# Kernel optimization log

Hardware: AMD Instinct MI355X
Metric: run time of the kernel (lower is better)

## Reference

```python
import jax, jax.numpy as jnp
import numpy as np

B, N, H, L = 4, 200, 128, 3
HH = H // 2
VOC_E_IN, VOC_E_OUT, NODE_DIM = 3, 2, 2
EPS_BN = 1e-5


def masked_bn(x, m, gamma, beta):
    """BatchNorm1d (batch stats, no running stats) applied only to masked positions.
    x: (..., H), m: (...) float mask. Unmasked entries pass through unchanged."""
    mm = m[..., None]
    cnt = jnp.sum(m)
    axes = tuple(range(x.ndim - 1))
    mean = jnp.sum(x * mm, axis=axes) / cnt
    var = jnp.sum(((x - mean) ** 2) * mm, axis=axes) / cnt  # biased, as BatchNorm1d
    xn = (x - mean) * jax.lax.rsqrt(var + EPS_BN) * gamma + beta
    return jnp.where(mm > 0, xn, x)


def gcn_layer(x, e, mask, sq_mask, p, i):
    # EdgeFeatures: e_ij = U*e_ij + V*x_i + V*x_j (V*x masked)
    Ue = jnp.einsum('bijh,hk->bijk', e, p['eU_w'][i]) + p['eU_b'][i]
    Vx_e = mask[..., None] * (jnp.einsum('bnh,hk->bnk', x, p['eV_w'][i]) + p['eV_b'][i])
    e_tmp = Ue + Vx_e[:, :, None, :] + Vx_e[:, None, :, :]
    gate = jax.nn.sigmoid(e_tmp)
    # NodeFeatures (mean aggregation)
    Ux = mask[..., None] * (jnp.einsum('bnh,hk->bnk', x, p['nU_w'][i]) + p['nU_b'][i])
    Vx = mask[..., None] * (jnp.einsum('bnh,hk->bnk', x, p['nV_w'][i]) + p['nV_b'][i])
    gate_m = gate * sq_mask[..., None]
    agg = jnp.einsum('bijh,bjh->bih', gate_m, Vx)
    denom = jnp.sum(gate_m, axis=2)
    x_tmp = Ux + agg / (1e-20 + denom)
    # masked batchnorm + ReLU + residual
    e_bn = masked_bn(e_tmp, sq_mask, p['bnE_g'][i], p['bnE_b'][i])
    x_bn = masked_bn(x_tmp, mask, p['bnN_g'][i], p['bnN_b'][i])
    return x + jax.nn.relu(x_bn), e + jax.nn.relu(e_bn)


def forward(x_edges, x_edges_values, x_nodes_coord, mask, p):
    x = jnp.einsum('bnd,dh->bnh', x_nodes_coord, p['w_coord'])          # (B,N,H)
    e_val = x_edges_values[..., None] * p['w_eval'][0]                  # (B,N,N,HH)
    e_tag = p['emb_edge'][x_edges]                                      # (B,N,N,HH)
    e = jnp.concatenate([e_val, e_tag], axis=-1)                        # (B,N,N,H)
    sq_mask = mask[:, :, None] * mask[:, None, :]
    for i in range(L):
        x, e = gcn_layer(x, e, mask, sq_mask, p, i)
    # MLP on edges (mlp_layers=2 -> one hidden ReLU layer)
    h = jax.nn.relu(jnp.einsum('bijh,hk->bijk', e, p['mlp_U_w']) + p['mlp_U_b'])
    y = jnp.einsum('bijh,hk->bijk', h, p['mlp_V_w']) + p['mlp_V_b']     # (B,N,N,2)
    return y


def setup_inputs() -> dict:
    key = jax.random.key(0)
    ks = jax.random.split(key, 32)
    x_edges = jax.random.randint(ks[0], (B, N, N), 0, VOC_E_IN)
    x_edges_values = jax.random.uniform(ks[1], (B, N, N), dtype=jnp.float32)
    x_nodes_coord = jax.random.uniform(ks[2], (B, N, NODE_DIM), dtype=jnp.float32)
    # prefix mask: variable graph sizes padded to N (as ConvTSP builds)
    lens = jax.random.randint(ks[3], (B,), N // 2, N + 1)
    mask = (jnp.arange(N)[None, :] < lens[:, None]).astype(jnp.float32)
    s = 1.0 / np.sqrt(H)
    inp = dict(x_edges=x_edges, x_edges_values=x_edges_values,
               x_nodes_coord=x_nodes_coord, mask=mask,
               w_coord=jax.random.normal(ks[4], (NODE_DIM, H)) * 0.5,
               w_eval=jax.random.normal(ks[5], (1, HH)) * 0.5,
               emb_edge=jax.random.normal(ks[6], (VOC_E_IN, HH)) * 0.5,
               eU_w=jax.random.normal(ks[7], (L, H, H)) * s,
               eU_b=jnp.zeros((L, H)),
               eV_w=jax.random.normal(ks[8], (L, H, H)) * s,
               eV_b=jnp.zeros((L, H)),
               nU_w=jax.random.normal(ks[9], (L, H, H)) * s,
               nU_b=jnp.zeros((L, H)),
               nV_w=jax.random.normal(ks[10], (L, H, H)) * s,
               nV_b=jnp.zeros((L, H)),
               bnE_g=jnp.ones((L, H)), bnE_b=jnp.zeros((L, H)),
               bnN_g=jnp.ones((L, H)), bnN_b=jnp.zeros((L, H)),
               mlp_U_w=jax.random.normal(ks[11], (H, H)) * s,
               mlp_U_b=jnp.zeros((H,)),
               mlp_V_w=jax.random.normal(ks[12], (H, VOC_E_OUT)) * s,
               mlp_V_b=jnp.zeros((VOC_E_OUT,)))
    return inp


def reference(x_edges, x_edges_values, x_nodes_coord, mask,
              w_coord, w_eval, emb_edge,
              eU_w, eU_b, eV_w, eV_b, nU_w, nU_b, nV_w, nV_b,
              bnE_g, bnE_b, bnN_g, bnN_b,
              mlp_U_w, mlp_U_b, mlp_V_w, mlp_V_b):
    p = dict(w_coord=w_coord, w_eval=w_eval, emb_edge=emb_edge,
             eU_w=eU_w, eU_b=eU_b, eV_w=eV_w, eV_b=eV_b,
             nU_w=nU_w, nU_b=nU_b, nV_w=nV_w, nV_b=nV_b,
             bnE_g=bnE_g, bnE_b=bnE_b, bnN_g=bnN_g, bnN_b=bnN_b,
             mlp_U_w=mlp_U_w, mlp_U_b=mlp_U_b, mlp_V_w=mlp_V_w, mlp_V_b=mlp_V_b)
    return forward(x_edges, x_edges_values, x_nodes_coord, mask, p)
```

## Files before the change

kernel.cpp:

```cpp
#include <hip/hip_runtime.h>
#include <hip/hip_bf16.h>


typedef __hip_bfloat16 bf16;
typedef __attribute__((ext_vector_type(8))) short short8_t;
typedef __attribute__((ext_vector_type(4))) float f32x4;

#define B_ 4
#define N_ 200
#define H_ 128
#define BN_ (B_ * N_)
#define MT_ 13
#define MROWS_ 208

__device__ __forceinline__ unsigned short f2b(float f) {
  unsigned int i = __float_as_uint(f);
  i = (i + 0x7fffu + ((i >> 16) & 1u)) >> 16;
  return (unsigned short)i;
}
__device__ __forceinline__ float b2f16(unsigned short u) {
  return __uint_as_float((unsigned int)u << 16);
}


__global__ __launch_bounds__(128) void k_init_x(
    const float* __restrict__ coord, const float* __restrict__ w_coord,
    float* __restrict__ x) {
  int bi = blockIdx.x, h = threadIdx.x;
  float c0 = coord[bi * 2 + 0], c1 = coord[bi * 2 + 1];
  x[(size_t)bi * H_ + h] = c0 * w_coord[h] + c1 * w_coord[H_ + h];
}

__global__ __launch_bounds__(256) void k_cnt(const float* __restrict__ mask,
                                             float* __restrict__ cnts) {
  int t = threadIdx.x, b = t >> 6, l = t & 63;
  float s = 0.f;
  for (int n = l; n < N_; n += 64) s += mask[b * N_ + n];
#pragma unroll
  for (int d = 1; d < 64; d <<= 1) s += __shfl_xor(s, d);
  __shared__ float ms[B_];
  if (l == 0) ms[b] = s;
  __syncthreads();
  if (t == 0) {
    float cn = 0.f, ce = 0.f;
    for (int k = 0; k < B_; ++k) { cn += ms[k]; ce += ms[k] * ms[k]; }
    cnts[0] = cn; cnts[1] = ce;
  }
}

__global__ __launch_bounds__(256) void k_prep_w(const float* __restrict__ eUw,
                                                const float* __restrict__ mUw,
                                                bf16* __restrict__ WT) {
  int blk = blockIdx.x;
  const float* src = (blk < 3) ? (eUw + (size_t)blk * H_ * H_) : mUw;
  bf16* dst = WT + (size_t)blk * H_ * H_;
  for (int q = threadIdx.x; q < H_ * H_; q += 256) {
    int out = q >> 7, in = q & 127;
    dst[q] = __float2bfloat16(src[in * H_ + out]);
  }
}


template <int UPD>
__global__ __launch_bounds__(128) void k_node_lin(
    float* __restrict__ x, const float* __restrict__ xtmp,
    const float* __restrict__ sumsPrev, const float* __restrict__ cnts,
    const float* __restrict__ gNp, const float* __restrict__ bNp,
    const float* __restrict__ eVw, const float* __restrict__ eVb,
    const float* __restrict__ nUw, const float* __restrict__ nUb,
    const float* __restrict__ nVw, const float* __restrict__ nVb,
    const float* __restrict__ mask, float* __restrict__ Vxe,
    float* __restrict__ Ux, float* __restrict__ Vx) {
  __shared__ float xr[H_];
  int bi = blockIdx.x, h = threadIdx.x;
  float m = mask[bi];
  float xv = x[(size_t)bi * H_ + h];
  if (UPD) {
    float cntN = cnts[0];
    float mN = sumsPrev[256 + h] / cntN;
    float vN = sumsPrev[384 + h] / cntN - mN * mN;
    float scN = gNp[h] * rsqrtf(vN + 1e-5f);
    float shN = bNp[h] - mN * scN;
    float tv = xtmp[(size_t)bi * H_ + h];
    float xn = (m > 0.f) ? fmaf(tv, scN, shN) : tv;
    xv += fmaxf(xn, 0.f);
    x[(size_t)bi * H_ + h] = xv;
  }
  xr[h] = xv;
  __syncthreads();
  float a = 0.f, bvv = 0.f, c = 0.f;
#pragma unroll 4
  for (int k = 0; k < H_; ++k) {
    float kx = xr[k];
    a   = fmaf(kx, eVw[k * H_ + h], a);
    bvv = fmaf(kx, nUw[k * H_ + h], bvv);
    c   = fmaf(kx, nVw[k * H_ + h], c);
  }
  Vxe[(size_t)bi * H_ + h] = m * (a + eVb[h]);
  Ux[(size_t)bi * H_ + h]  = m * (bvv + nUb[h]);
  Vx[(size_t)bi * H_ + h]  = m * (c + nVb[h]);
}


template <int MODE, bool DO_X>
__global__ __launch_bounds__(256, 3) void k_edge(
    bf16* __restrict__ e, bf16* __restrict__ etmp,
    const float* __restrict__ sumsPrev, const float* __restrict__ cnts,
    const float* __restrict__ gEp, const float* __restrict__ bEp,
    const int* __restrict__ xe, const float* __restrict__ ev,
    const float* __restrict__ w_eval, const float* __restrict__ emb,
    const bf16* __restrict__ WT, const float* __restrict__ eUb,
    const float* __restrict__ Vxe, const float* __restrict__ Vx,
    const float* __restrict__ Ux, const float* __restrict__ mask,
    float* __restrict__ xtmp, float* __restrict__ sumsCur) {
  __shared__ __align__(16) char sA[MROWS_ * 256];
  __shared__ float ssE_s[256];
  const int bi = blockIdx.x;
  const int b = bi / N_;
  const int t = threadIdx.x;
  const int lane = t & 63;
  const int w = t >> 6;
  const float mask_i = mask[bi];

  if (MODE != 0) {
    int h = t & 127;
    float cntE = cnts[1];
    float mE = sumsPrev[h] / cntE;
    float vE = sumsPrev[128 + h] / cntE - mE * mE;
    float scE = gEp[h] * rsqrtf(vE + 1e-5f);
    ssE_s[t] = (t < 128) ? scE : (bEp[h] - mE * scE);
    __syncthreads();
  }

  const int colA = (w << 5) + (lane & 15);
  const int colB = colA + 16;
  const int kgrp = (lane >> 4) << 3;
  const short* wp0 = (const short*)WT + colA * H_ + kgrp;
  const short* wp1 = (const short*)WT + colB * H_ + kgrp;
  short8_t bfA0 = *(const short8_t*)(wp0);
  short8_t bfA1 = *(const short8_t*)(wp0 + 32);
  short8_t bfA2 = *(const short8_t*)(wp0 + 64);
  short8_t bfA3 = *(const short8_t*)(wp0 + 96);
  short8_t bfB0 = *(const short8_t*)(wp1);
  short8_t bfB1 = *(const short8_t*)(wp1 + 32);
  short8_t bfB2 = *(const short8_t*)(wp1 + 64);
  short8_t bfB3 = *(const short8_t*)(wp1 + 96);

  {
    unsigned short* eb = (unsigned short*)e + (size_t)bi * N_ * H_;
    const unsigned short* tb =
        (const unsigned short*)etmp + (size_t)bi * N_ * H_;
    for (int q4 = t; q4 < MROWS_ * 32; q4 += 256) {
      int row = q4 >> 5, k0 = (q4 & 31) << 2;
      float v0 = 0.f, v1 = 0.f, v2 = 0.f, v3 = 0.f;
      if (row < N_) {
        if (MODE == 0 || MODE == 2) {
          if (k0 < 64) {
            float evv = ev[bi * N_ + row];
            float4 we = *(const float4*)(w_eval + k0);
            v0 = evv * we.x; v1 = evv * we.y;
            v2 = evv * we.z; v3 = evv * we.w;
          } else {
            float4 em4 = *(const float4*)(emb + xe[bi * N_ + row] * 64 + (k0 - 64));
            v0 = em4.x; v1 = em4.y; v2 = em4.z; v3 = em4.w;
          }
        } else {
          ushort4 e4 = *(const ushort4*)(eb + row * H_ + k0);
          v0 = b2f16(e4.x); v1 = b2f16(e4.y);
          v2 = b2f16(e4.z); v3 = b2f16(e4.w);
        }
        if (MODE != 0) {
          ushort4 t4 = *(const ushort4*)(tb + row * H_ + k0);
          float mj = mask[b * N_ + row];
          bool msk = (mask_i * mj) > 0.f;
          float sc0 = ssE_s[k0 + 0], sc1 = ssE_s[k0 + 1];
          float sc2 = ssE_s[k0 + 2], sc3 = ssE_s[k0 + 3];
          float sh0 = ssE_s[128 + k0 + 0], sh1 = ssE_s[128 + k0 + 1];
          float sh2 = ssE_s[128 + k0 + 2], sh3 = ssE_s[128 + k0 + 3];
          float f0 = b2f16(t4.x), f1 = b2f16(t4.y);
          float f2 = b2f16(t4.z), f3 = b2f16(t4.w);
          v0 += fmaxf(msk ? fmaf(f0, sc0, sh0) : f0, 0.f);
          v1 += fmaxf(msk ? fmaf(f1, sc1, sh1) : f1, 0.f);
          v2 += fmaxf(msk ? fmaf(f2, sc2, sh2) : f2, 0.f);
          v3 += fmaxf(msk ? fmaf(f3, sc3, sh3) : f3, 0.f);
        }
      }
      unsigned int p0 = ((unsigned int)f2b(v1) << 16) | f2b(v0);
      unsigned int p1 = ((unsigned int)f2b(v3) << 16) | f2b(v2);
      if (MODE != 0 && row < N_)
        *(uint2*)(eb + row * H_ + k0) = make_uint2(p0, p1);
      unsigned long long pk = ((unsigned long long)p1 << 32) | p0;
      int byo = (row << 8) + ((k0 * 2) ^ ((row & 7) << 4));
      *(unsigned long long*)(sA + byo) = pk;
    }
  }
  __syncthreads();

  const float add0 = eUb[colA] + Vxe[(size_t)bi * H_ + colA];
  const float add1 = eUb[colB] + Vxe[(size_t)bi * H_ + colB];
  const float* VxeB = Vxe + (size_t)b * N_ * H_;
  const float* VxB  = Vx  + (size_t)b * N_ * H_;

  float agg0 = 0.f, agg1 = 0.f, den0 = 0.f, den1 = 0.f;
  float s1a = 0.f, s1b = 0.f, s2a = 0.f, s2b = 0.f;
  const int kb = (lane >> 4) << 4;

  for (int mt = 0; mt < MT_; ++mt) {
    f32x4 acc0 = {0.f, 0.f, 0.f, 0.f}, acc1 = {0.f, 0.f, 0.f, 0.f};
    int ra = (mt << 4) + (lane & 15);
    const char* ap = sA + (ra << 8);
    int sw = (ra & 7) << 4;
    short8_t av;
    av = *(const short8_t*)(ap + ((kb + 0) ^ sw));
    acc0 = __builtin_amdgcn_mfma_f32_16x16x32_bf16(av, bfA0, acc0, 0, 0, 0);
    acc1 = __builtin_amdgcn_mfma_f32_16x16x32_bf16(av, bfB0, acc1, 0, 0, 0);
    av = *(const short8_t*)(ap + ((kb + 64) ^ sw));
    acc0 = __builtin_amdgcn_mfma_f32_16x16x32_bf16(av, bfA1, acc0, 0, 0, 0);
    acc1 = __builtin_amdgcn_mfma_f32_16x16x32_bf16(av, bfB1, acc1, 0, 0, 0);
    av = *(const short8_t*)(ap + ((kb + 128) ^ sw));
    acc0 = __builtin_amdgcn_mfma_f32_16x16x32_bf16(av, bfA2, acc0, 0, 0, 0);
    acc1 = __builtin_amdgcn_mfma_f32_16x16x32_bf16(av, bfB2, acc1, 0, 0, 0);
    av = *(const short8_t*)(ap + ((kb + 192) ^ sw));
    acc0 = __builtin_amdgcn_mfma_f32_16x16x32_bf16(av, bfA3, acc0, 0, 0, 0);
    acc1 = __builtin_amdgcn_mfma_f32_16x16x32_bf16(av, bfB3, acc1, 0, 0, 0);
#pragma unroll
    for (int r = 0; r < 4; ++r) {
      int j = (mt << 4) + ((lane >> 4) << 2) + r;
      bool valid = (j < N_);
      float mj = valid ? mask[b * N_ + j] : 0.f;
      float sqm = mask_i * mj;
      float vj0 = valid ? VxeB[(size_t)j * H_ + colA] : 0.f;
      float vj1 = valid ? VxeB[(size_t)j * H_ + colB] : 0.f;
      float t0 = acc0[r] + add0 + vj0;
      float t1 = acc1[r] + add1 + vj1;
      if (valid) {
        size_t o = ((size_t)bi * N_ + j) * H_;
        ((unsigned short*)etmp)[o + colA] = f2b(t0);
        ((unsigned short*)etmp)[o + colB] = f2b(t1);
      }
      float g0 = sqm / (1.f + __expf(-t0));
      float g1 = sqm / (1.f + __expf(-t1));
      float vx0 = valid ? VxB[(size_t)j * H_ + colA] : 0.f;
      float vx1 = valid ? VxB[(size_t)j * H_ + colB] : 0.f;
      agg0 = fmaf(g0, vx0, agg0);
      agg1 = fmaf(g1, vx1, agg1);
      den0 += g0; den1 += g1;
      s1a = fmaf(t0, sqm, s1a);
      s1b = fmaf(t1, sqm, s1b);
      s2a = fmaf(t0 * sqm, t0, s2a);
      s2b = fmaf(t1 * sqm, t1, s2b);
    }
  }
#pragma unroll
  for (int d = 16; d <= 32; d <<= 1) {
    agg0 += __shfl_xor(agg0, d); agg1 += __shfl_xor(agg1, d);
    den0 += __shfl_xor(den0, d); den1 += __shfl_xor(den1, d);
    s1a += __shfl_xor(s1a, d);   s1b += __shfl_xor(s1b, d);
    s2a += __shfl_xor(s2a, d);   s2b += __shfl_xor(s2b, d);
  }
  if ((lane >> 4) == 0) {
    atomicAdd(&sumsCur[colA], s1a);
    atomicAdd(&sumsCur[colB], s1b);
    atomicAdd(&sumsCur[128 + colA], s2a);
    atomicAdd(&sumsCur[128 + colB], s2b);
    if (DO_X) {
      float xt0 = Ux[(size_t)bi * H_ + colA] + agg0 / (1e-20f + den0);
      float xt1 = Ux[(size_t)bi * H_ + colB] + agg1 / (1e-20f + den1);
      xtmp[(size_t)bi * H_ + colA] = xt0;
      xtmp[(size_t)bi * H_ + colB] = xt1;
      atomicAdd(&sumsCur[256 + colA], xt0 * mask_i);
      atomicAdd(&sumsCur[384 + colA], xt0 * xt0 * mask_i);
      atomicAdd(&sumsCur[256 + colB], xt1 * mask_i);
      atomicAdd(&sumsCur[384 + colB], xt1 * xt1 * mask_i);
    }
  }
}


__global__ __launch_bounds__(256, 2) void k_head(
    const bf16* __restrict__ e, const bf16* __restrict__ etmp,
    const float* __restrict__ sumsPrev, const float* __restrict__ cnts,
    const float* __restrict__ gEp, const float* __restrict__ bEp,
    const bf16* __restrict__ UT, const float* __restrict__ Ub,
    const float* __restrict__ Vw, const float* __restrict__ Vb,
    const float* __restrict__ mask, float* __restrict__ y) {
  __shared__ __align__(16) char sA[MROWS_ * 256];
  __shared__ float part[4][MROWS_][2];
  __shared__ float ssE_s[256];
  const int bi = blockIdx.x;
  const int b = bi / N_;
  const int t = threadIdx.x;
  const int lane = t & 63;
  const int w = t >> 6;
  const float mask_i = mask[bi];

  {
    int h = t & 127;
    float cntE = cnts[1];
    float mE = sumsPrev[h] / cntE;
    float vE = sumsPrev[128 + h] / cntE - mE * mE;
    float scE = gEp[h] * rsqrtf(vE + 1e-5f);
    ssE_s[t] = (t < 128) ? scE : (bEp[h] - mE * scE);
    __syncthreads();
  }

  const int colA = (w << 5) + (lane & 15);
  const int colB = colA + 16;
  const int kgrp = (lane >> 4) << 3;
  const short* wp0 = (const short*)UT + colA * H_ + kgrp;
  const short* wp1 = (const short*)UT + colB * H_ + kgrp;
  short8_t bfA0 = *(const short8_t*)(wp0);
  short8_t bfA1 = *(const short8_t*)(wp0 + 32);
  short8_t bfA2 = *(const short8_t*)(wp0 + 64);
  short8_t bfA3 = *(const short8_t*)(wp0 + 96);
  short8_t bfB0 = *(const short8_t*)(wp1);
  short8_t bfB1 = *(const short8_t*)(wp1 + 32);
  short8_t bfB2 = *(const short8_t*)(wp1 + 64);
  short8_t bfB3 = *(const short8_t*)(wp1 + 96);

  {
    const unsigned short* eb = (const unsigned short*)e + (size_t)bi * N_ * H_;
    const unsigned short* tb =
        (const unsigned short*)etmp + (size_t)bi * N_ * H_;
    for (int q4 = t; q4 < MROWS_ * 32; q4 += 256) {
      int row = q4 >> 5, k0 = (q4 & 31) << 2;
      float v0 = 0.f, v1 = 0.f, v2 = 0.f, v3 = 0.f;
      if (row < N_) {
        ushort4 e4 = *(const ushort4*)(eb + row * H_ + k0);
        ushort4 t4 = *(const ushort4*)(tb + row * H_ + k0);
        float mj = mask[b * N_ + row];
        bool msk = (mask_i * mj) > 0.f;
        float sc0 = ssE_s[k0 + 0], sc1 = ssE_s[k0 + 1];
        float sc2 = ssE_s[k0 + 2], sc3 = ssE_s[k0 + 3];
        float sh0 = ssE_s[128 + k0 + 0], sh1 = ssE_s[128 + k0 + 1];
        float sh2 = ssE_s[128 + k0 + 2], sh3 = ssE_s[128 + k0 + 3];
        float f0 = b2f16(t4.x), f1 = b2f16(t4.y);
        float f2 = b2f16(t4.z), f3 = b2f16(t4.w);
        v0 = b2f16(e4.x) + fmaxf(msk ? fmaf(f0, sc0, sh0) : f0, 0.f);
        v1 = b2f16(e4.y) + fmaxf(msk ? fmaf(f1, sc1, sh1) : f1, 0.f);
        v2 = b2f16(e4.z) + fmaxf(msk ? fmaf(f2, sc2, sh2) : f2, 0.f);
        v3 = b2f16(e4.w) + fmaxf(msk ? fmaf(f3, sc3, sh3) : f3, 0.f);
      }
      unsigned int p0 = ((unsigned int)f2b(v1) << 16) | f2b(v0);
      unsigned int p1 = ((unsigned int)f2b(v3) << 16) | f2b(v2);
      unsigned long long pk = ((unsigned long long)p1 << 32) | p0;
      int byo = (row << 8) + ((k0 * 2) ^ ((row & 7) << 4));
      *(unsigned long long*)(sA + byo) = pk;
    }
  }
  __syncthreads();

  float bu0 = Ub[colA], bu1 = Ub[colB];
  float v00 = Vw[colA * 2], v01 = Vw[colA * 2 + 1];
  float v10 = Vw[colB * 2], v11 = Vw[colB * 2 + 1];
  const int kb = (lane >> 4) << 4;

  for (int mt = 0; mt < MT_; ++mt) {
    f32x4 acc0 = {0.f, 0.f, 0.f, 0.f}, acc1 = {0.f, 0.f, 0.f, 0.f};
    int ra = (mt << 4) + (lane & 15);
    const char* ap = sA + (ra << 8);
    int sw = (ra & 7) << 4;
    short8_t av;
    av = *(const short8_t*)(ap + ((kb + 0) ^ sw));
    acc0 = __builtin_amdgcn_mfma_f32_16x16x32_bf16(av, bfA0, acc0, 0, 0, 0);
    acc1 = __builtin_amdgcn_mfma_f32_16x16x32_bf16(av, bfB0, acc1, 0, 0, 0);
    av = *(const short8_t*)(ap + ((kb + 64) ^ sw));
    acc0 = __builtin_amdgcn_mfma_f32_16x16x32_bf16(av, bfA1, acc0, 0, 0, 0);
    acc1 = __builtin_amdgcn_mfma_f32_16x16x32_bf16(av, bfB1, acc1, 0, 0, 0);
    av = *(const short8_t*)(ap + ((kb + 128) ^ sw));
    acc0 = __builtin_amdgcn_mfma_f32_16x16x32_bf16(av, bfA2, acc0, 0, 0, 0);
    acc1 = __builtin_amdgcn_mfma_f32_16x16x32_bf16(av, bfB2, acc1, 0, 0, 0);
    av = *(const short8_t*)(ap + ((kb + 192) ^ sw));
    acc0 = __builtin_amdgcn_mfma_f32_16x16x32_bf16(av, bfA3, acc0, 0, 0, 0);
    acc1 = __builtin_amdgcn_mfma_f32_16x16x32_bf16(av, bfB3, acc1, 0, 0, 0);
#pragma unroll
    for (int r = 0; r < 4; ++r) {
      float h0v = fmaxf(acc0[r] + bu0, 0.f);
      float h1v = fmaxf(acc1[r] + bu1, 0.f);
      float p0 = h0v * v00 + h1v * v10;
      float p1 = h0v * v01 + h1v * v11;
#pragma unroll
      for (int d = 1; d < 16; d <<= 1) {
        p0 += __shfl_xor(p0, d);
        p1 += __shfl_xor(p1, d);
      }
      int jl = (mt << 4) + ((lane >> 4) << 2) + r;
      if ((lane & 15) == 0) { part[w][jl][0] = p0; part[w][jl][1] = p1; }
    }
  }
  __syncthreads();
  float vb0 = Vb[0], vb1 = Vb[1];
  for (int q = t; q < N_ * 2; q += 256) {
    int j = q >> 1, c = q & 1;
    float s = part[0][j][c] + part[1][j][c] + part[2][j][c] + part[3][j][c] +
              (c ? vb1 : vb0);
    y[((size_t)bi * N_ + j) * 2 + c] = s;
  }
}


extern "C" void kernel_launch(void* const* d_in, const int* in_sizes, int n_in,
                              void* d_out, int out_size, void* d_ws,
                              size_t ws_size, hipStream_t stream) {
  const int*   x_edges = (const int*)d_in[0];
  const float* ev      = (const float*)d_in[1];
  const float* coord   = (const float*)d_in[2];
  const float* mask    = (const float*)d_in[3];
  const float* w_coord = (const float*)d_in[4];
  const float* w_eval  = (const float*)d_in[5];
  const float* emb     = (const float*)d_in[6];
  const float* eUw = (const float*)d_in[7];
  const float* eUb = (const float*)d_in[8];
  const float* eVw = (const float*)d_in[9];
  const float* eVb = (const float*)d_in[10];
  const float* nUw = (const float*)d_in[11];
  const float* nUb = (const float*)d_in[12];
  const float* nVw = (const float*)d_in[13];
  const float* nVb = (const float*)d_in[14];
  const float* gE  = (const float*)d_in[15];
  const float* bE  = (const float*)d_in[16];
  const float* gN  = (const float*)d_in[17];
  const float* bN  = (const float*)d_in[18];
  const float* mUw = (const float*)d_in[19];
  const float* mUb = (const float*)d_in[20];
  const float* mVw = (const float*)d_in[21];
  const float* mVb = (const float*)d_in[22];

  char* ws = (char*)d_ws;
  size_t off = 0;
  auto alloc = [&](size_t bytes) {
    void* p = ws + off;
    off += (bytes + 255) & ~(size_t)255;
    return p;
  };
  bf16* e     = (bf16*)alloc((size_t)B_ * N_ * N_ * H_ * 2);
  bf16* etmp  = (bf16*)alloc((size_t)B_ * N_ * N_ * H_ * 2);
  float* x    = (float*)alloc((size_t)BN_ * H_ * 4);
  float* Vxe  = (float*)alloc((size_t)BN_ * H_ * 4);
  float* Ux   = (float*)alloc((size_t)BN_ * H_ * 4);
  float* Vx   = (float*)alloc((size_t)BN_ * H_ * 4);
  float* xtmp = (float*)alloc((size_t)BN_ * H_ * 4);
  float* sums = (float*)alloc(3 * 512 * 4);
  float* cnts = (float*)alloc(256);
  bf16* WT    = (bf16*)alloc((size_t)4 * H_ * H_ * 2);

  hipMemsetAsync(sums, 0, 3 * 512 * 4, stream);
  k_prep_w<<<4, 256, 0, stream>>>(eUw, mUw, WT);
  k_init_x<<<BN_, 128, 0, stream>>>(coord, w_coord, x);
  k_cnt<<<1, 256, 0, stream>>>(mask, cnts);

  float* sums0 = sums;
  float* sums1 = sums + 512;
  float* sums2 = sums + 1024;

  k_node_lin<0><<<BN_, 128, 0, stream>>>(
      x, xtmp, sums0, cnts, gN, bN, eVw, eVb, nUw, nUb, nVw, nVb, mask, Vxe,
      Ux, Vx);
  k_edge<0, true><<<BN_, 256, 0, stream>>>(
      e, etmp, sums0, cnts, gE, bE, x_edges, ev, w_eval, emb, WT, eUb, Vxe,
      Vx, Ux, mask, xtmp, sums0);
  k_node_lin<1><<<BN_, 128, 0, stream>>>(
      x, xtmp, sums0, cnts, gN, bN, eVw + H_ * H_, eVb + H_, nUw + H_ * H_,
      nUb + H_, nVw + H_ * H_, nVb + H_, mask, Vxe, Ux, Vx);
  k_edge<2, true><<<BN_, 256, 0, stream>>>(
      e, etmp, sums0, cnts, gE, bE, x_edges, ev, w_eval, emb, WT + H_ * H_,
      eUb + H_, Vxe, Vx, Ux, mask, xtmp, sums1);
  k_node_lin<1><<<BN_, 128, 0, stream>>>(
      x, xtmp, sums1, cnts, gN + H_, bN + H_, eVw + 2 * H_ * H_,
      eVb + 2 * H_, nUw + 2 * H_ * H_, nUb + 2 * H_, nVw + 2 * H_ * H_,
      nVb + 2 * H_, mask, Vxe, Ux, Vx);
  k_edge<1, false><<<BN_, 256, 0, stream>>>(
      e, etmp, sums1, cnts, gE + H_, bE + H_, x_edges, ev, w_eval, emb,
      WT + 2 * H_ * H_, eUb + 2 * H_, Vxe, Vx, Ux, mask, xtmp, sums2);
  k_head<<<BN_, 256, 0, stream>>>(e, etmp, sums2, cnts, gE + 2 * H_,
                                  bE + 2 * H_, WT + (size_t)3 * H_ * H_, mUb,
                                  mVw, mVb, mask, (float*)d_out);
}
```

Measured before the change: 384.6 us.

## Split edge and head kernels over four j-tiles with partial-sum reduction kernels

```diff
diff --git a/kernel.cpp b/kernel.cpp
--- a/kernel.cpp
+++ b/kernel.cpp
@@ -10,8 +10,9 @@
 #define N_ 200
 #define H_ 128
 #define BN_ (B_ * N_)
-#define MT_ 13
-#define MROWS_ 208
+#define JT_ 4
+#define NBLK_ (BN_ * JT_)
+#define MAXROWS_ 64
 
 __device__ __forceinline__ unsigned short f2b(float f) {
   unsigned int i = __float_as_uint(f);
@@ -111,11 +112,14 @@
     const float* __restrict__ w_eval, const float* __restrict__ emb,
     const bf16* __restrict__ WT, const float* __restrict__ eUb,
     const float* __restrict__ Vxe, const float* __restrict__ Vx,
-    const float* __restrict__ Ux, const float* __restrict__ mask,
-    float* __restrict__ xtmp, float* __restrict__ sumsCur) {
-  __shared__ __align__(16) char sA[MROWS_ * 256];
+    const float* __restrict__ mask, float* __restrict__ pS,
+    float* __restrict__ pAgg, float* __restrict__ pDen) {
+  __shared__ __align__(16) char sA[MAXROWS_ * 256];
   __shared__ float ssE_s[256];
-  const int bi = blockIdx.x;
+  const int bi = blockIdx.x >> 2;
+  const int jh = blockIdx.x & 3;
+  const int mt0 = (jh == 0) ? 0 : 3 * jh + 1;
+  const int mt1 = 3 * jh + 4;
   const int b = bi / N_;
   const int t = threadIdx.x;
   const int lane = t & 63;
@@ -147,11 +151,13 @@
   short8_t bfB3 = *(const short8_t*)(wp1 + 96);
 
   {
+    const int nrt = (mt1 - mt0) << 4;
     unsigned short* eb = (unsigned short*)e + (size_t)bi * N_ * H_;
     const unsigned short* tb =
         (const unsigned short*)etmp + (size_t)bi * N_ * H_;
-    for (int q4 = t; q4 < MROWS_ * 32; q4 += 256) {
-      int row = q4 >> 5, k0 = (q4 & 31) << 2;
+    for (int q4 = t; q4 < nrt * 32; q4 += 256) {
+      int lr = q4 >> 5, k0 = (q4 & 31) << 2;
+      int row = (mt0 << 4) + lr;
       float v0 = 0.f, v1 = 0.f, v2 = 0.f, v3 = 0.f;
       if (row < N_) {
         if (MODE == 0 || MODE == 2) {
@@ -190,7 +196,7 @@
       if (MODE != 0 && row < N_)
         *(uint2*)(eb + row * H_ + k0) = make_uint2(p0, p1);
       unsigned long long pk = ((unsigned long long)p1 << 32) | p0;
-      int byo = (row << 8) + ((k0 * 2) ^ ((row & 7) << 4));
+      int byo = (lr << 8) + ((k0 * 2) ^ ((lr & 7) << 4));
       *(unsigned long long*)(sA + byo) = pk;
     }
   }
@@ -205,9 +211,9 @@
   float s1a = 0.f, s1b = 0.f, s2a = 0.f, s2b = 0.f;
   const int kb = (lane >> 4) << 4;
 
-  for (int mt = 0; mt < MT_; ++mt) {
+  for (int mt = mt0; mt < mt1; ++mt) {
     f32x4 acc0 = {0.f, 0.f, 0.f, 0.f}, acc1 = {0.f, 0.f, 0.f, 0.f};
-    int ra = (mt << 4) + (lane & 15);
+    int ra = ((mt - mt0) << 4) + (lane & 15);
     const char* ap = sA + (ra << 8);
     int sw = (ra & 7) << 4;
     short8_t av;
@@ -259,35 +265,78 @@
     s2a += __shfl_xor(s2a, d);   s2b += __shfl_xor(s2b, d);
   }
   if ((lane >> 4) == 0) {
-    atomicAdd(&sumsCur[colA], s1a);
-    atomicAdd(&sumsCur[colB], s1b);
-    atomicAdd(&sumsCur[128 + colA], s2a);
-    atomicAdd(&sumsCur[128 + colB], s2b);
+    float* ps = pS + (size_t)blockIdx.x * 256;
+    ps[colA] = s1a;
+    ps[colB] = s1b;
+    ps[128 + colA] = s2a;
+    ps[128 + colB] = s2b;
     if (DO_X) {
-      float xt0 = Ux[(size_t)bi * H_ + colA] + agg0 / (1e-20f + den0);
-      float xt1 = Ux[(size_t)bi * H_ + colB] + agg1 / (1e-20f + den1);
-      xtmp[(size_t)bi * H_ + colA] = xt0;
-      xtmp[(size_t)bi * H_ + colB] = xt1;
-      atomicAdd(&sumsCur[256 + colA], xt0 * mask_i);
-      atomicAdd(&sumsCur[384 + colA], xt0 * xt0 * mask_i);
-      atomicAdd(&sumsCur[256 + colB], xt1 * mask_i);
-      atomicAdd(&sumsCur[384 + colB], xt1 * xt1 * mask_i);
-    }
-  }
-}
-
-
-__global__ __launch_bounds__(256, 2) void k_head(
+      size_t po = ((size_t)jh * BN_ + bi) * H_;
+      pAgg[po + colA] = agg0;
+      pAgg[po + colB] = agg1;
+      pDen[po + colA] = den0;
+      pDen[po + colB] = den1;
+    }
+  }
+}
+
+
+__global__ __launch_bounds__(128) void k_xfin(
+    const float* __restrict__ pAgg, const float* __restrict__ pDen,
+    const float* __restrict__ Ux, float* __restrict__ xtmp) {
+  int bi = blockIdx.x, h = threadIdx.x;
+  float a0 = pAgg[(size_t)bi * H_ + h];
+  float a1 = pAgg[((size_t)BN_ + bi) * H_ + h];
+  float a2 = pAgg[((size_t)2 * BN_ + bi) * H_ + h];
+  float a3 = pAgg[((size_t)3 * BN_ + bi) * H_ + h];
+  float d0 = pDen[(size_t)bi * H_ + h];
+  float d1 = pDen[((size_t)BN_ + bi) * H_ + h];
+  float d2 = pDen[((size_t)2 * BN_ + bi) * H_ + h];
+  float d3 = pDen[((size_t)3 * BN_ + bi) * H_ + h];
+  float a = (a0 + a1) + (a2 + a3);
+  float d = (d0 + d1) + (d2 + d3);
+  xtmp[(size_t)bi * H_ + h] = Ux[(size_t)bi * H_ + h] + a / (1e-20f + d);
+}
+
+
+__global__ __launch_bounds__(256) void k_red(
+    const float* __restrict__ pS, const float* __restrict__ xtmp,
+    const float* __restrict__ mask, float* __restrict__ sums, int doN) {
+  int g = blockIdx.x, t = threadIdx.x;
+  if (g < 32) {
+    float acc = 0.f;
+    for (int blk = g * (NBLK_ / 32); blk < (g + 1) * (NBLK_ / 32); ++blk)
+      acc += pS[(size_t)blk * 256 + t];
+    atomicAdd(&sums[t], acc);
+  } else if (doN) {
+    int g2 = g - 32;
+    int col = t & 127;
+    bool sq = t >= 128;
+    float acc = 0.f;
+    for (int bi = g2 * (BN_ / 32); bi < (g2 + 1) * (BN_ / 32); ++bi) {
+      float mi = mask[bi];
+      float xt = xtmp[(size_t)bi * H_ + col];
+      acc += (sq ? xt * xt : xt) * mi;
+    }
+    atomicAdd(&sums[256 + t], acc);
+  }
+}
+
+
+__global__ __launch_bounds__(256, 3) void k_head(
     const bf16* __restrict__ e, const bf16* __restrict__ etmp,
     const float* __restrict__ sumsPrev, const float* __restrict__ cnts,
     const float* __restrict__ gEp, const float* __restrict__ bEp,
     const bf16* __restrict__ UT, const float* __restrict__ Ub,
     const float* __restrict__ Vw, const float* __restrict__ Vb,
     const float* __restrict__ mask, float* __restrict__ y) {
-  __shared__ __align__(16) char sA[MROWS_ * 256];
-  __shared__ float part[4][MROWS_][2];
+  __shared__ __align__(16) char sA[MAXROWS_ * 256];
+  __shared__ float part[4][MAXROWS_][2];
   __shared__ float ssE_s[256];
-  const int bi = blockIdx.x;
+  const int bi = blockIdx.x >> 2;
+  const int jh = blockIdx.x & 3;
+  const int mt0 = (jh == 0) ? 0 : 3 * jh + 1;
+  const int mt1 = 3 * jh + 4;
   const int b = bi / N_;
   const int t = threadIdx.x;
   const int lane = t & 63;
@@ -319,11 +368,13 @@
   short8_t bfB3 = *(const short8_t*)(wp1 + 96);
 
   {
+    const int nrt = (mt1 - mt0) << 4;
     const unsigned short* eb = (const unsigned short*)e + (size_t)bi * N_ * H_;
     const unsigned short* tb =
         (const unsigned short*)etmp + (size_t)bi * N_ * H_;
-    for (int q4 = t; q4 < MROWS_ * 32; q4 += 256) {
-      int row = q4 >> 5, k0 = (q4 & 31) << 2;
+    for (int q4 = t; q4 < nrt * 32; q4 += 256) {
+      int lr = q4 >> 5, k0 = (q4 & 31) << 2;
+      int row = (mt0 << 4) + lr;
       float v0 = 0.f, v1 = 0.f, v2 = 0.f, v3 = 0.f;
       if (row < N_) {
         ushort4 e4 = *(const ushort4*)(eb + row * H_ + k0);
@@ -344,7 +395,7 @@
       unsigned int p0 = ((unsigned int)f2b(v1) << 16) | f2b(v0);
       unsigned int p1 = ((unsigned int)f2b(v3) << 16) | f2b(v2);
       unsigned long long pk = ((unsigned long long)p1 << 32) | p0;
-      int byo = (row << 8) + ((k0 * 2) ^ ((row & 7) << 4));
+      int byo = (lr << 8) + ((k0 * 2) ^ ((lr & 7) << 4));
       *(unsigned long long*)(sA + byo) = pk;
     }
   }
@@ -355,9 +406,9 @@
   float v10 = Vw[colB * 2], v11 = Vw[colB * 2 + 1];
   const int kb = (lane >> 4) << 4;
 
-  for (int mt = 0; mt < MT_; ++mt) {
+  for (int mt = mt0; mt < mt1; ++mt) {
     f32x4 acc0 = {0.f, 0.f, 0.f, 0.f}, acc1 = {0.f, 0.f, 0.f, 0.f};
-    int ra = (mt << 4) + (lane & 15);
+    int ra = ((mt - mt0) << 4) + (lane & 15);
     const char* ap = sA + (ra << 8);
     int sw = (ra & 7) << 4;
     short8_t av;
@@ -384,17 +435,21 @@
         p0 += __shfl_xor(p0, d);
         p1 += __shfl_xor(p1, d);
       }
-      int jl = (mt << 4) + ((lane >> 4) << 2) + r;
+      int jl = ((mt - mt0) << 4) + ((lane >> 4) << 2) + r;
       if ((lane & 15) == 0) { part[w][jl][0] = p0; part[w][jl][1] = p1; }
     }
   }
   __syncthreads();
   float vb0 = Vb[0], vb1 = Vb[1];
-  for (int q = t; q < N_ * 2; q += 256) {
-    int j = q >> 1, c = q & 1;
-    float s = part[0][j][c] + part[1][j][c] + part[2][j][c] + part[3][j][c] +
-              (c ? vb1 : vb0);
-    y[((size_t)bi * N_ + j) * 2 + c] = s;
+  const int nrt = (mt1 - mt0) << 4;
+  for (int q = t; q < nrt * 2; q += 256) {
+    int jl = q >> 1, c = q & 1;
+    int j = (mt0 << 4) + jl;
+    if (j < N_) {
+      float s = part[0][jl][c] + part[1][jl][c] + part[2][jl][c] +
+                part[3][jl][c] + (c ? vb1 : vb0);
+      y[((size_t)bi * N_ + j) * 2 + c] = s;
+    }
   }
 }
 
@@ -440,6 +495,9 @@
   float* Ux   = (float*)alloc((size_t)BN_ * H_ * 4);
   float* Vx   = (float*)alloc((size_t)BN_ * H_ * 4);
   float* xtmp = (float*)alloc((size_t)BN_ * H_ * 4);
+  float* pS   = (float*)alloc((size_t)NBLK_ * 256 * 4);
+  float* pAgg = (float*)alloc((size_t)JT_ * BN_ * H_ * 4);
+  float* pDen = (float*)alloc((size_t)JT_ * BN_ * H_ * 4);
   float* sums = (float*)alloc(3 * 512 * 4);
   float* cnts = (float*)alloc(256);
   bf16* WT    = (bf16*)alloc((size_t)4 * H_ * H_ * 2);
@@ -456,23 +514,28 @@
   k_node_lin<0><<<BN_, 128, 0, stream>>>(
       x, xtmp, sums0, cnts, gN, bN, eVw, eVb, nUw, nUb, nVw, nVb, mask, Vxe,
       Ux, Vx);
-  k_edge<0, true><<<BN_, 256, 0, stream>>>(
+  k_edge<0, true><<<NBLK_, 256, 0, stream>>>(
       e, etmp, sums0, cnts, gE, bE, x_edges, ev, w_eval, emb, WT, eUb, Vxe,
-      Vx, Ux, mask, xtmp, sums0);
+      Vx, mask, pS, pAgg, pDen);
+  k_xfin<<<BN_, 128, 0, stream>>>(pAgg, pDen, Ux, xtmp);
+  k_red<<<64, 256, 0, stream>>>(pS, xtmp, mask, sums0, 1);
   k_node_lin<1><<<BN_, 128, 0, stream>>>(
       x, xtmp, sums0, cnts, gN, bN, eVw + H_ * H_, eVb + H_, nUw + H_ * H_,
       nUb + H_, nVw + H_ * H_, nVb + H_, mask, Vxe, Ux, Vx);
-  k_edge<2, true><<<BN_, 256, 0, stream>>>(
+  k_edge<2, true><<<NBLK_, 256, 0, stream>>>(
       e, etmp, sums0, cnts, gE, bE, x_edges, ev, w_eval, emb, WT + H_ * H_,
-      eUb + H_, Vxe, Vx, Ux, mask, xtmp, sums1);
+      eUb + H_, Vxe, Vx, mask, pS, pAgg, pDen);
+  k_xfin<<<BN_, 128, 0, stream>>>(pAgg, pDen, Ux, xtmp);
+  k_red<<<64, 256, 0, stream>>>(pS, xtmp, mask, sums1, 1);
   k_node_lin<1><<<BN_, 128, 0, stream>>>(
       x, xtmp, sums1, cnts, gN + H_, bN + H_, eVw + 2 * H_ * H_,
       eVb + 2 * H_, nUw + 2 * H_ * H_, nUb + 2 * H_, nVw + 2 * H_ * H_,
       nVb + 2 * H_, mask, Vxe, Ux, Vx);
-  k_edge<1, false><<<BN_, 256, 0, stream>>>(
+  k_edge<1, false><<<NBLK_, 256, 0, stream>>>(
       e, etmp, sums1, cnts, gE + H_, bE + H_, x_edges, ev, w_eval, emb,
-      WT + 2 * H_ * H_, eUb + 2 * H_, Vxe, Vx, Ux, mask, xtmp, sums2);
-  k_head<<<BN_, 256, 0, stream>>>(e, etmp, sums2, cnts, gE + 2 * H_,
-                                  bE + 2 * H_, WT + (size_t)3 * H_ * H_, mUb,
-                                  mVw, mVb, mask, (float*)d_out);
-}
+      WT + 2 * H_ * H_, eUb + 2 * H_, Vxe, Vx, mask, pS, pAgg, pDen);
+  k_red<<<64, 256, 0, stream>>>(pS, xtmp, mask, sums2, 0);
+  k_head<<<NBLK_, 256, 0, stream>>>(e, etmp, sums2, cnts, gE + 2 * H_,
+                                    bE + 2 * H_, WT + (size_t)3 * H_ * H_,
+                                    mUb, mVw, mVb, mask, (float*)d_out);
+}
```

After: 346.6 us. -9.9%, faster.
